# Kernel optimization log

Measured on AMD Instinct MI355X. Metric: run time of the kernel, lower is better.

## Reference

```python
import jax, jax.numpy as jnp
import numpy as np

EPS = 1e-5
NUM_HEADS = 8
KEY_DIM = 32
V_DIM = 128  # att_ratio * key_dim

def bn2d(x, g, b, m, v):
    # inference BatchNorm2d on NCHW
    s = g * jax.lax.rsqrt(v + EPS)
    return x * s[None, :, None, None] + (b - m * s)[None, :, None, None]

def conv1x1(x, w):
    # w: [out_c, in_c], x: [B,C,H,W]
    return jnp.einsum('oc,bchw->bohw', w, x)

def _bn_params(key, c):
    k1, k2, k3, k4 = jax.random.split(key, 4)
    g = jax.random.uniform(k1, (c,), jnp.float32, 0.5, 1.5)
    b = jax.random.normal(k2, (c,), jnp.float32) * 0.1
    m = jax.random.normal(k3, (c,), jnp.float32) * 0.1
    v = jax.random.uniform(k4, (c,), jnp.float32, 0.5, 1.5)
    return g, b, m, v

def setup_inputs() -> dict:
    key = jax.random.key(0)
    ks = jax.random.split(key, 12)
    inp_dim, out_dim = 256, 512
    kv_out = (KEY_DIM + V_DIM) * NUM_HEADS      # 1280
    q_out = KEY_DIM * NUM_HEADS                 # 256
    merge_dim = V_DIM * NUM_HEADS               # 1024
    hid = out_dim * 2                            # mlp_ratio=2 -> 1024
    d = {}
    d['x'] = jax.random.normal(ks[0], (32, inp_dim, 32, 32), jnp.float32)
    d['kv_w'] = jax.random.normal(ks[1], (kv_out, inp_dim), jnp.float32) * 0.02
    d['kv_g'], d['kv_b'], d['kv_m'], d['kv_v'] = _bn_params(ks[2], kv_out)
    d['q_w'] = jax.random.normal(ks[3], (q_out, inp_dim), jnp.float32) * 0.02
    d['q_g'], d['q_b'], d['q_m'], d['q_v'] = _bn_params(ks[4], q_out)
    d['mg_w'] = jax.random.normal(ks[5], (out_dim, merge_dim), jnp.float32) * 0.02
    d['mg_g'], d['mg_b'], d['mg_m'], d['mg_v'] = _bn_params(ks[6], out_dim)
    d['fc1_w'] = jax.random.normal(ks[7], (hid, out_dim), jnp.float32) * 0.02
    d['bn1_g'], d['bn1_b'], d['bn1_m'], d['bn1_v'] = _bn_params(ks[8], hid)
    d['fc2_w'] = jax.random.normal(ks[9], (out_dim, hid), jnp.float32) * 0.02
    d['bn2_g'], d['bn2_b'], d['bn2_m'], d['bn2_v'] = _bn_params(ks[10], out_dim)
    return d

def reference(x, kv_w, kv_g, kv_b, kv_m, kv_v, q_w, q_g, q_b, q_m, q_v,
              mg_w, mg_g, mg_b, mg_m, mg_v,
              fc1_w, bn1_g, bn1_b, bn1_m, bn1_v,
              fc2_w, bn2_g, bn2_b, bn2_m, bn2_v):
    B, C, H, W = x.shape
    scale = KEY_DIM ** (-0.5)
    # kv projection: conv1x1 + BN, then split per head into k, v
    kv = bn2d(conv1x1(x, kv_w), kv_g, kv_b, kv_m, kv_v)
    kv = kv.reshape(B, NUM_HEADS, KEY_DIM + V_DIM, H * W)
    k = kv[:, :, :KEY_DIM]   # [B,h,Dk,N]
    v = kv[:, :, KEY_DIM:]   # [B,h,Dv,N]
    # query subsampling: AvgPool2d(kernel=1, stride=2) == strided slice
    xq = x[:, :, ::2, ::2]
    q = bn2d(conv1x1(xq, q_w), q_g, q_b, q_m, q_v)
    q = q.reshape(B, NUM_HEADS, KEY_DIM, -1)  # [B,h,Dk,Nq]
    # att = q^T @ k * scale, softmax over keys
    att = jax.nn.softmax(jnp.einsum('bhdq,bhdn->bhqn', q, k) * scale, axis=-1)
    h2, w2 = (H + 1) // 2, (W + 1) // 2
    # out = v @ att^T, channel-first layout
    o = jnp.einsum('bhvn,bhqn->bhvq', v, att).reshape(B, NUM_HEADS * V_DIM, h2, w2)
    # merge: GELU -> conv1x1 -> BN
    o = bn2d(conv1x1(jax.nn.gelu(o, approximate=False), mg_w), mg_g, mg_b, mg_m, mg_v)
    # ConvMlp: conv1x1 -> BN -> GELU -> conv1x1 -> BN
    y = bn2d(conv1x1(o, fc1_w), bn1_g, bn1_b, bn1_m, bn1_v)
    y = jax.nn.gelu(y, approximate=False)
    y = bn2d(conv1x1(y, fc2_w), bn2_g, bn2_b, bn2_m, bn2_v)
    return y
```

## Files before the change

kernel.cpp:

```cpp
#include <hip/hip_runtime.h>
#include <hip/hip_bf16.h>

#define BN_EPS 1e-5f

typedef short s8v __attribute__((ext_vector_type(8)));
typedef float f4v __attribute__((ext_vector_type(4)));
typedef unsigned short u16x8 __attribute__((ext_vector_type(8)));

__device__ __forceinline__ float bu2f(unsigned short u) {
    union { unsigned int i; float f; } c; c.i = ((unsigned int)u) << 16; return c.f;
}
__device__ __forceinline__ unsigned short f2bu(float f) {
    union { float f; unsigned int i; } c; c.f = f;
    unsigned int i = c.i;
    i += 0x7FFFu + ((i >> 16) & 1u);
    return (unsigned short)(i >> 16);
}
__device__ __forceinline__ float gelu_exact(float x) {
    return 0.5f * x * (1.0f + erff(x * 0.70710678118654752f));
}
__device__ __forceinline__ float ldin(const void* p, long i, bool f32) {
    return f32 ? ((const float*)p)[i] : bu2f(((const unsigned short*)p)[i]);
}
__device__ __forceinline__ s8v ldfrag(const unsigned short* p) {
    return *reinterpret_cast<const s8v*>(p);
}
__device__ __forceinline__ void gld16(const void* g, void* l) {
    __builtin_amdgcn_global_load_lds(
        (const __attribute__((address_space(1))) unsigned int*)g,
        (__attribute__((address_space(3))) unsigned int*)l, 16, 0, 0);
}
__device__ __forceinline__ s8v ldsw32(const unsigned short* T, int row, int quad) {
    return *reinterpret_cast<const s8v*>(T + row * 32 + ((quad ^ ((row >> 1) & 3)) << 3));
}
__device__ __forceinline__ s8v ldsw64(const unsigned short* T, int row, int chunk) {
    return *reinterpret_cast<const s8v*>(T + row * 64 + ((chunk ^ (row & 7)) << 3));
}
__device__ __forceinline__ int detect_f32(const unsigned short* xu) {
    int insane = 0;
    for (int i = 0; i < 128; ++i) {
        unsigned int e = (xu[i] >> 7) & 0xFFu;
        if (e == 255u || (e != 0u && (e < 96u || e > 159u))) ++insane;
    }
    return (insane >= 16) ? 1 : 0;
}

__global__ __launch_bounds__(256)
void prep_kernel(const void* __restrict__ x,
                 const void* __restrict__ w0, const void* __restrict__ w1,
                 const void* __restrict__ w2, const void* __restrict__ w3,
                 const void* __restrict__ w4,
                 unsigned short* __restrict__ wdst,
                 unsigned short* __restrict__ xT,
                 unsigned short* __restrict__ xqT,
                 int* __restrict__ dtf)
{
    __shared__ int sflag;
    __shared__ unsigned short T[64][66];
    const int tid = threadIdx.x;
    const int bid = blockIdx.x;
    if (tid == 0) {
        int fl = detect_f32((const unsigned short*)x);
        sflag = fl;
        if (bid == 0) *dtf = fl;
    }
    __syncthreads();
    const bool f = (sflag != 0);

    if (bid < 960) {
        long idx = (long)bid * 2048 + tid * 8;
        const void* s; long off;
        if      (idx <  327680L) { s = w0; off = idx; }
        else if (idx <  393216L) { s = w1; off = idx - 327680L; }
        else if (idx <  917504L) { s = w2; off = idx - 393216L; }
        else if (idx < 1441792L) { s = w3; off = idx - 917504L; }
        else                     { s = w4; off = idx - 1441792L; }
        u16x8 pk;
        if (f) {
            float4 a = *((const float4*)((const float*)s + off));
            float4 b = *((const float4*)((const float*)s + off + 4));
            pk[0]=f2bu(a.x); pk[1]=f2bu(a.y); pk[2]=f2bu(a.z); pk[3]=f2bu(a.w);
            pk[4]=f2bu(b.x); pk[5]=f2bu(b.y); pk[6]=f2bu(b.z); pk[7]=f2bu(b.w);
        } else {
            pk = *((const u16x8*)((const unsigned short*)s + off));
        }
        *reinterpret_cast<u16x8*>(wdst + idx) = pk;
        return;
    }
    int b, c0, n0, ND; bool SUBS;
    if (bid < 3008) { int t = bid - 960;  b = t >> 6; int r = t & 63;
                      c0 = (r >> 4) * 64; n0 = (r & 15) * 64; ND = 1024; SUBS = false; }
    else            { int t = bid - 3008; b = t >> 4; int r = t & 15;
                      c0 = (r >> 2) * 64; n0 = (r & 3) * 64;  ND = 256;  SUBS = true; }
    unsigned short* dst = SUBS ? xqT : xT;
    {
        int nn = tid & 63, cq = tid >> 6;
        int n = n0 + nn;
        int sc = SUBS ? ((n >> 4) * 64 + (n & 15) * 2) : n;
        long base = ((long)b * 256 + c0 + cq * 16) * 1024 + sc;
        #pragma unroll
        for (int i = 0; i < 16; ++i)
            T[nn][cq * 16 + i] = f2bu(ldin(x, base + (long)i * 1024, f));
    }
    __syncthreads();
    {
        int cc = tid & 63, nq = tid >> 6;
        #pragma unroll
        for (int i = 0; i < 16; ++i) {
            int nn = nq * 16 + i;
            dst[((long)b * ND + n0 + nn) * 256 + c0 + cc] = T[nn][cc];
        }
    }
}

template<int OUT_MODE, bool DO_GELU, bool PRESCALE, int BM>
__global__ __launch_bounds__(256)
void mfma_gemm(const unsigned short* __restrict__ A,
               const unsigned short* __restrict__ B,
               const void* __restrict__ gg, const void* __restrict__ bb,
               const void* __restrict__ mmu, const void* __restrict__ vv,
               void* __restrict__ out0, unsigned short* __restrict__ out1,
               int M, int K, int N, const int* __restrict__ dtflag)
{
    constexpr int NF = (BM == 128) ? 4 : 2;
    __shared__ unsigned short As[BM * 64];
    __shared__ unsigned short Bs[128 * 64];
    __shared__ float sS[BM], sO[BM];

    const bool wf = (*dtflag != 0);
    const int tid = threadIdx.x;
    const int lane = tid & 63;
    const int wave = tid >> 6;
    const int quad = lane >> 4;
    const int l15  = lane & 15;
    const int wm2 = (BM == 128) ? (wave >> 1) * 64 : 0;
    const int wn2 = (BM == 128) ? (wave & 1) * 64 : wave * 32;
    const int b  = blockIdx.z;
    const int bm = blockIdx.y * BM;
    const int bn = blockIdx.x * 128;

    if (tid < BM) {
        int m = bm + tid;
        float g  = ldin(gg,  m, wf), be = ldin(bb,  m, wf);
        float mu = ldin(mmu, m, wf), va = ldin(vv,  m, wf);
        float s = g * rsqrtf(va + BN_EPS);
        float o = be - mu * s;
        if (PRESCALE) { s *= 0.17677669529663687f; o *= 0.17677669529663687f; }
        sS[tid] = s; sO[tid] = o;
    }

    const unsigned short* Bb = B + (long)b * N * K;

    f4v acc[4][NF];
    #pragma unroll
    for (int i = 0; i < 4; ++i)
        #pragma unroll
        for (int j = 0; j < NF; ++j) acc[i][j] = (f4v){0.f, 0.f, 0.f, 0.f};

    const int lr8 = lane >> 3;
    const int lc8 = lane & 7;

    for (int k0 = 0; k0 < K; k0 += 64) {
        #pragma unroll
        for (int j = 0; j < (BM == 128 ? 4 : 2); ++j) {
            int base = wave * (BM == 128 ? 32 : 16) + j * 8;
            int r = base + lr8;
            gld16(A + (long)(bm + r) * K + k0 + ((lc8 ^ (r & 7)) << 3),
                  As + base * 64);
        }
        #pragma unroll
        for (int j = 0; j < 4; ++j) {
            int base = wave * 32 + j * 8;
            int r = base + lr8;
            gld16(Bb + (long)(bn + r) * K + k0 + ((lc8 ^ (r & 7)) << 3),
                  Bs + base * 64);
        }
        __syncthreads();

        #pragma unroll
        for (int sk = 0; sk < 2; ++sk) {
            s8v af[4], bfr[NF];
            #pragma unroll
            for (int i = 0; i < 4; ++i)
                af[i]  = ldsw64(As, wm2 + i * 16 + l15, sk * 4 + quad);
            #pragma unroll
            for (int j = 0; j < NF; ++j)
                bfr[j] = ldsw64(Bs, wn2 + j * 16 + l15, sk * 4 + quad);
            #pragma unroll
            for (int i = 0; i < 4; ++i)
                #pragma unroll
                for (int j = 0; j < NF; ++j)
                    acc[i][j] = __builtin_amdgcn_mfma_f32_16x16x32_bf16(
                        af[i], bfr[j], acc[i][j], 0, 0, 0);
        }
        __syncthreads();
    }

    #pragma unroll
    for (int i = 0; i < 4; ++i) {
        int m0l = wm2 + i * 16 + quad * 4;
        int m0  = bm + m0l;
        float s0 = sS[m0l + 0], o0 = sO[m0l + 0];
        float s1 = sS[m0l + 1], o1 = sO[m0l + 1];
        float s2 = sS[m0l + 2], o2 = sO[m0l + 2];
        float s3 = sS[m0l + 3], o3 = sO[m0l + 3];
        #pragma unroll
        for (int j = 0; j < NF; ++j) {
            int n = bn + wn2 + j * 16 + l15;
            float v0 = acc[i][j][0] * s0 + o0;
            float v1 = acc[i][j][1] * s1 + o1;
            float v2 = acc[i][j][2] * s2 + o2;
            float v3 = acc[i][j][3] * s3 + o3;
            if (DO_GELU) {
                v0 = gelu_exact(v0); v1 = gelu_exact(v1);
                v2 = gelu_exact(v2); v3 = gelu_exact(v3);
            }
            if (OUT_MODE == 0) {
                ushort4 pk; pk.x = f2bu(v0); pk.y = f2bu(v1);
                pk.z = f2bu(v2); pk.w = f2bu(v3);
                *reinterpret_cast<ushort4*>(
                    (unsigned short*)out0 + ((long)b * N + n) * M + m0) = pk;
            } else if (OUT_MODE == 1) {
                int h = m0 / 160, seg = m0 - h * 160;
                if (seg < 32) {
                    ushort4 pk; pk.x = f2bu(v0); pk.y = f2bu(v1);
                    pk.z = f2bu(v2); pk.w = f2bu(v3);
                    *reinterpret_cast<ushort4*>(
                        (unsigned short*)out0 + ((long)(b * 8 + h) * 1024 + n) * 32 + seg) = pk;
                } else {
                    long vb = (((long)b * 8 + h) * 128 + (seg - 32)) * N + n;
                    out1[vb + 0 * N] = f2bu(v0);
                    out1[vb + 1 * N] = f2bu(v1);
                    out1[vb + 2 * N] = f2bu(v2);
                    out1[vb + 3 * N] = f2bu(v3);
                }
            } else if (OUT_MODE == 2) {
                int b2 = n >> 8, nl = n & 255;
                long ob = ((long)b2 * M + m0) * 256 + nl;
                if (wf) {
                    ((float*)out0)[ob + 0L * 256] = v0;
                    ((float*)out0)[ob + 1L * 256] = v1;
                    ((float*)out0)[ob + 2L * 256] = v2;
                    ((float*)out0)[ob + 3L * 256] = v3;
                } else {
                    ((unsigned short*)out0)[ob + 0L * 256] = f2bu(v0);
                    ((unsigned short*)out0)[ob + 1L * 256] = f2bu(v1);
                    ((unsigned short*)out0)[ob + 2L * 256] = f2bu(v2);
                    ((unsigned short*)out0)[ob + 3L * 256] = f2bu(v3);
                }
            } else {
                int h = m0 >> 5;
                ushort4 pk; pk.x = f2bu(v0); pk.y = f2bu(v1);
                pk.z = f2bu(v2); pk.w = f2bu(v3);
                *reinterpret_cast<ushort4*>(
                    (unsigned short*)out0 + ((long)(b * 8 + h) * 256 + n) * 32 + (m0 & 31)) = pk;
            }
        }
    }
}

__global__ __launch_bounds__(512, 4)
void attn_mfma(const unsigned short* __restrict__ kvK,
               const unsigned short* __restrict__ kvV,
               const unsigned short* __restrict__ qh,
               unsigned short* __restrict__ goT)
{
    __shared__ unsigned short Ks[64 * 32];
    __shared__ unsigned short Vs[128 * 64];
    __shared__ unsigned short Ps[128][72];
    __shared__ float redS[128];

    const int tid = threadIdx.x;
    const int lane = tid & 63;
    const int wave = tid >> 6;
    const int quad = lane >> 4;
    const int l15  = lane & 15;
    const int h    = blockIdx.x;
    const int b    = blockIdx.y;
    const int q0   = blockIdx.z * 128;
    const int wq   = wave * 16;

    const unsigned short* Qb = qh  + (long)(b * 8 + h) * 256 * 32;
    const unsigned short* Kb = kvK + (long)(b * 8 + h) * 1024 * 32;
    const unsigned short* Vb = kvV + (long)(b * 8 + h) * 128 * 1024;

    s8v qf = ldfrag(Qb + (long)(q0 + wq + l15) * 32 + quad * 8);

    f4v o[8];
    #pragma unroll
    for (int i = 0; i < 8; ++i) o[i] = (f4v){0.f, 0.f, 0.f, 0.f};
    float rs[4] = {0.f, 0.f, 0.f, 0.f};

    for (int n0 = 0; n0 < 1024; n0 += 64) {
        if (wave < 4) {
            int r = wave * 16 + (lane >> 2);
            int c = (lane & 3) ^ ((r >> 1) & 3);
            gld16(Kb + (long)(n0 + r) * 32 + (c << 3), Ks + wave * 16 * 32);
        }
        {
            int rb = wave * 16;
            int r0 = rb + (lane >> 3), r1 = r0 + 8;
            int s  = lane & 7;
            gld16(Vb + (long)r0 * 1024 + n0 + ((s ^ (r0 & 7)) << 3), Vs + rb * 64);
            gld16(Vb + (long)r1 * 1024 + n0 + ((s ^ (r1 & 7)) << 3), Vs + (rb + 8) * 64);
        }
        __syncthreads();

        #pragma unroll
        for (int j = 0; j < 4; ++j) {
            s8v kf = ldsw32(Ks, j * 16 + l15, quad);
            f4v z = (f4v){0.f, 0.f, 0.f, 0.f};
            f4v sa = __builtin_amdgcn_mfma_f32_16x16x32_bf16(qf, kf, z, 0, 0, 0);
            #pragma unroll
            for (int r = 0; r < 4; ++r) {
                float p = __expf(fminf(sa[r], 30.f));
                rs[r] += p;
                Ps[wq + quad * 4 + r][j * 16 + l15] = f2bu(p);
            }
        }
        #pragma unroll
        for (int ks = 0; ks < 2; ++ks) {
            s8v pf = ldfrag(&Ps[wq + l15][ks * 32 + quad * 8]);
            #pragma unroll
            for (int i = 0; i < 8; ++i) {
                s8v vf = ldsw64(Vs, i * 16 + l15, ks * 4 + quad);
                o[i] = __builtin_amdgcn_mfma_f32_16x16x32_bf16(vf, pf, o[i], 0, 0, 0);
            }
        }
        __syncthreads();
    }

    #pragma unroll
    for (int r = 0; r < 4; ++r) {
        float s = rs[r];
        s += __shfl_xor(s, 1);
        s += __shfl_xor(s, 2);
        s += __shfl_xor(s, 4);
        s += __shfl_xor(s, 8);
        if (l15 == 0) redS[wq + quad * 4 + r] = s;
    }
    float linv = 1.0f / redS[wq + l15];
    int q = q0 + wq + l15;
    #pragma unroll
    for (int i = 0; i < 8; ++i) {
        ushort4 pk;
        pk.x = f2bu(gelu_exact(o[i][0] * linv));
        pk.y = f2bu(gelu_exact(o[i][1] * linv));
        pk.z = f2bu(gelu_exact(o[i][2] * linv));
        pk.w = f2bu(gelu_exact(o[i][3] * linv));
        *reinterpret_cast<ushort4*>(
            goT + ((long)b * 256 + q) * 1024 + h * 128 + i * 16 + quad * 4) = pk;
    }
}

extern "C" void kernel_launch(void* const* d_in, const int* in_sizes, int n_in,
                              void* d_out, int out_size, void* d_ws, size_t ws_size,
                              hipStream_t stream)
{
    const void* x     = d_in[0];
    const void* kv_w  = d_in[1];
    const void* kv_g  = d_in[2];  const void* kv_b  = d_in[3];
    const void* kv_m  = d_in[4];  const void* kv_v  = d_in[5];
    const void* q_w   = d_in[6];
    const void* q_g   = d_in[7];  const void* q_b   = d_in[8];
    const void* q_m   = d_in[9];  const void* q_v   = d_in[10];
    const void* mg_w  = d_in[11];
    const void* mg_g  = d_in[12]; const void* mg_b  = d_in[13];
    const void* mg_m  = d_in[14]; const void* mg_v  = d_in[15];
    const void* fc1_w = d_in[16];
    const void* bn1_g = d_in[17]; const void* bn1_b = d_in[18];
    const void* bn1_m = d_in[19]; const void* bn1_v = d_in[20];
    const void* fc2_w = d_in[21];
    const void* bn2_g = d_in[22]; const void* bn2_b = d_in[23];
    const void* bn2_m = d_in[24]; const void* bn2_v = d_in[25];

    unsigned short* ws  = (unsigned short*)d_ws;
    int*            dtf = (int*)d_ws;
    unsigned short* wsW  = ws + 8;
    unsigned short* wKV  = wsW;
    unsigned short* wQ   = wsW + 327680L;
    unsigned short* wMG  = wsW + 393216L;
    unsigned short* wFC1 = wsW + 917504L;
    unsigned short* wFC2 = wsW + 1441792L;
    unsigned short* xT   = ws + 1966088L;
    unsigned short* goT  = xT;
    unsigned short* xqT  = ws + 10354696L;
    unsigned short* qhb  = ws + 12451848L;
    unsigned short* kvK  = ws + 14549000L;
    unsigned short* kvV  = ws + 22937608L;
    unsigned short* y1T  = kvV;
    unsigned short* y2T  = kvV + 4194304L;

    dim3 blk(256, 1, 1);

    prep_kernel<<<3520, blk, 0, stream>>>(
        x, kv_w, q_w, mg_w, fc1_w, fc2_w, wsW, xT, xqT, dtf);

    mfma_gemm<3, false, true, 64><<<dim3(2, 4, 32), blk, 0, stream>>>(
        wQ, xqT, q_g, q_b, q_m, q_v, qhb, nullptr, 256, 256, 256, dtf);

    mfma_gemm<1, false, false, 128><<<dim3(8, 10, 32), blk, 0, stream>>>(
        wKV, xT, kv_g, kv_b, kv_m, kv_v, kvK, kvV, 1280, 256, 1024, dtf);

    attn_mfma<<<dim3(8, 32, 2), dim3(512, 1, 1), 0, stream>>>(kvK, kvV, qhb, goT);

    mfma_gemm<0, false, false, 64><<<dim3(64, 8, 1), blk, 0, stream>>>(
        wMG, goT, mg_g, mg_b, mg_m, mg_v, y1T, nullptr, 512, 1024, 8192, dtf);

    mfma_gemm<0, true, false, 64><<<dim3(64, 16, 1), blk, 0, stream>>>(
        wFC1, y1T, bn1_g, bn1_b, bn1_m, bn1_v, y2T, nullptr, 1024, 512, 8192, dtf);

    mfma_gemm<2, false, false, 64><<<dim3(64, 8, 1), blk, 0, stream>>>(
        wFC2, y2T, bn2_g, bn2_b, bn2_m, bn2_v, d_out, nullptr, 512, 1024, 8192, dtf);
}
```

Baseline: 307.8 us.

## Split KV projection into K and V GEMMs with LDS-staged coalesced stores

Reorders the KV weight rows during prep so all K rows and all V rows are contiguous. The KV projection then runs as two kernels: the K part uses the generic GEMM with remapped BN parameters, and a new V GEMM swaps operand roles and transposes its tile through LDS. Both write 16-byte coalesced rows, replacing the scalar strided V stores. The generic GEMM also stages its mode 0/3 epilogue through a shared-memory tile for wide stores, and sets a minimum occupancy hint. This adds a kernel launch and extra LDS traffic plus barriers in the epilogue.

```diff
diff --git a/kernel.cpp b/kernel.cpp
--- a/kernel.cpp
+++ b/kernel.cpp
@@ -70,7 +70,13 @@
     if (bid < 960) {
         long idx = (long)bid * 2048 + tid * 8;
         const void* s; long off;
-        if      (idx <  327680L) { s = w0; off = idx; }
+        if (idx < 65536L) {
+            long rk = idx >> 8;
+            s = w0; off = ((rk >> 5) * 160 + (rk & 31)) * 256 + (idx & 255);
+        } else if (idx < 327680L) {
+            long rv = (idx - 65536L) >> 8;
+            s = w0; off = ((rv >> 7) * 160 + 32 + (rv & 127)) * 256 + (idx & 255);
+        }
         else if (idx <  393216L) { s = w1; off = idx - 327680L; }
         else if (idx <  917504L) { s = w2; off = idx - 393216L; }
         else if (idx < 1441792L) { s = w3; off = idx - 917504L; }
@@ -113,19 +119,20 @@
     }
 }
 
-template<int OUT_MODE, bool DO_GELU, bool PRESCALE, int BM>
-__global__ __launch_bounds__(256)
+template<int OUT_MODE, bool DO_GELU, bool PRESCALE, bool REMAPK>
+__global__ __launch_bounds__(256, 4)
 void mfma_gemm(const unsigned short* __restrict__ A,
                const unsigned short* __restrict__ B,
                const void* __restrict__ gg, const void* __restrict__ bb,
                const void* __restrict__ mmu, const void* __restrict__ vv,
-               void* __restrict__ out0, unsigned short* __restrict__ out1,
+               void* __restrict__ out0,
                int M, int K, int N, const int* __restrict__ dtflag)
 {
-    constexpr int NF = (BM == 128) ? 4 : 2;
-    __shared__ unsigned short As[BM * 64];
-    __shared__ unsigned short Bs[128 * 64];
-    __shared__ float sS[BM], sO[BM];
+    __shared__ union {
+        struct { unsigned short As[64 * 64]; unsigned short Bs[128 * 64]; } s;
+        unsigned short tile[128 * 68];
+    } u;
+    __shared__ float sS[64], sO[64];
 
     const bool wf = (*dtflag != 0);
     const int tid = threadIdx.x;
@@ -133,16 +140,16 @@
     const int wave = tid >> 6;
     const int quad = lane >> 4;
     const int l15  = lane & 15;
-    const int wm2 = (BM == 128) ? (wave >> 1) * 64 : 0;
-    const int wn2 = (BM == 128) ? (wave & 1) * 64 : wave * 32;
+    const int wn2 = wave * 32;
     const int b  = blockIdx.z;
-    const int bm = blockIdx.y * BM;
+    const int bm = blockIdx.y * 64;
     const int bn = blockIdx.x * 128;
 
-    if (tid < BM) {
+    if (tid < 64) {
         int m = bm + tid;
-        float g  = ldin(gg,  m, wf), be = ldin(bb,  m, wf);
-        float mu = ldin(mmu, m, wf), va = ldin(vv,  m, wf);
+        int mo = REMAPK ? ((m >> 5) * 160 + (m & 31)) : m;
+        float g  = ldin(gg,  mo, wf), be = ldin(bb,  mo, wf);
+        float mu = ldin(mmu, mo, wf), va = ldin(vv,  mo, wf);
         float s = g * rsqrtf(va + BN_EPS);
         float o = be - mu * s;
         if (PRESCALE) { s *= 0.17677669529663687f; o *= 0.17677669529663687f; }
@@ -151,90 +158,101 @@
 
     const unsigned short* Bb = B + (long)b * N * K;
 
-    f4v acc[4][NF];
+    f4v acc[4][2];
     #pragma unroll
     for (int i = 0; i < 4; ++i)
         #pragma unroll
-        for (int j = 0; j < NF; ++j) acc[i][j] = (f4v){0.f, 0.f, 0.f, 0.f};
+        for (int j = 0; j < 2; ++j) acc[i][j] = (f4v){0.f, 0.f, 0.f, 0.f};
 
     const int lr8 = lane >> 3;
     const int lc8 = lane & 7;
 
     for (int k0 = 0; k0 < K; k0 += 64) {
         #pragma unroll
-        for (int j = 0; j < (BM == 128 ? 4 : 2); ++j) {
-            int base = wave * (BM == 128 ? 32 : 16) + j * 8;
+        for (int j = 0; j < 2; ++j) {
+            int base = wave * 16 + j * 8;
             int r = base + lr8;
             gld16(A + (long)(bm + r) * K + k0 + ((lc8 ^ (r & 7)) << 3),
-                  As + base * 64);
+                  u.s.As + base * 64);
         }
         #pragma unroll
         for (int j = 0; j < 4; ++j) {
             int base = wave * 32 + j * 8;
             int r = base + lr8;
             gld16(Bb + (long)(bn + r) * K + k0 + ((lc8 ^ (r & 7)) << 3),
-                  Bs + base * 64);
+                  u.s.Bs + base * 64);
         }
         __syncthreads();
 
         #pragma unroll
         for (int sk = 0; sk < 2; ++sk) {
-            s8v af[4], bfr[NF];
+            s8v af[4], bfr[2];
             #pragma unroll
             for (int i = 0; i < 4; ++i)
-                af[i]  = ldsw64(As, wm2 + i * 16 + l15, sk * 4 + quad);
-            #pragma unroll
-            for (int j = 0; j < NF; ++j)
-                bfr[j] = ldsw64(Bs, wn2 + j * 16 + l15, sk * 4 + quad);
+                af[i]  = ldsw64(u.s.As, i * 16 + l15, sk * 4 + quad);
+            #pragma unroll
+            for (int j = 0; j < 2; ++j)
+                bfr[j] = ldsw64(u.s.Bs, wn2 + j * 16 + l15, sk * 4 + quad);
             #pragma unroll
             for (int i = 0; i < 4; ++i)
                 #pragma unroll
-                for (int j = 0; j < NF; ++j)
+                for (int j = 0; j < 2; ++j)
                     acc[i][j] = __builtin_amdgcn_mfma_f32_16x16x32_bf16(
                         af[i], bfr[j], acc[i][j], 0, 0, 0);
         }
         __syncthreads();
     }
 
-    #pragma unroll
-    for (int i = 0; i < 4; ++i) {
-        int m0l = wm2 + i * 16 + quad * 4;
-        int m0  = bm + m0l;
-        float s0 = sS[m0l + 0], o0 = sO[m0l + 0];
-        float s1 = sS[m0l + 1], o1 = sO[m0l + 1];
-        float s2 = sS[m0l + 2], o2 = sO[m0l + 2];
-        float s3 = sS[m0l + 3], o3 = sO[m0l + 3];
-        #pragma unroll
-        for (int j = 0; j < NF; ++j) {
-            int n = bn + wn2 + j * 16 + l15;
-            float v0 = acc[i][j][0] * s0 + o0;
-            float v1 = acc[i][j][1] * s1 + o1;
-            float v2 = acc[i][j][2] * s2 + o2;
-            float v3 = acc[i][j][3] * s3 + o3;
-            if (DO_GELU) {
-                v0 = gelu_exact(v0); v1 = gelu_exact(v1);
-                v2 = gelu_exact(v2); v3 = gelu_exact(v3);
+    if (OUT_MODE == 0 || OUT_MODE == 3) {
+        #pragma unroll
+        for (int j = 0; j < 2; ++j) {
+            int n = wn2 + j * 16 + l15;
+            #pragma unroll
+            for (int i = 0; i < 4; ++i) {
+                int mcol = i * 16 + quad * 4;
+                ushort4 pk;
+                float v0 = acc[i][j][0] * sS[mcol + 0] + sO[mcol + 0];
+                float v1 = acc[i][j][1] * sS[mcol + 1] + sO[mcol + 1];
+                float v2 = acc[i][j][2] * sS[mcol + 2] + sO[mcol + 2];
+                float v3 = acc[i][j][3] * sS[mcol + 3] + sO[mcol + 3];
+                if (DO_GELU) {
+                    v0 = gelu_exact(v0); v1 = gelu_exact(v1);
+                    v2 = gelu_exact(v2); v3 = gelu_exact(v3);
+                }
+                pk.x = f2bu(v0); pk.y = f2bu(v1); pk.z = f2bu(v2); pk.w = f2bu(v3);
+                *reinterpret_cast<ushort4*>(&u.tile[n * 68 + mcol]) = pk;
             }
+        }
+        __syncthreads();
+        #pragma unroll
+        for (int p = 0; p < 4; ++p) {
+            int n = p * 32 + (tid >> 3), c = tid & 7;
+            u16x8 val = *reinterpret_cast<const u16x8*>(&u.tile[n * 68 + c * 8]);
             if (OUT_MODE == 0) {
-                ushort4 pk; pk.x = f2bu(v0); pk.y = f2bu(v1);
-                pk.z = f2bu(v2); pk.w = f2bu(v3);
-                *reinterpret_cast<ushort4*>(
-                    (unsigned short*)out0 + ((long)b * N + n) * M + m0) = pk;
-            } else if (OUT_MODE == 1) {
-                int h = m0 / 160, seg = m0 - h * 160;
-                if (seg < 32) {
-                    ushort4 pk; pk.x = f2bu(v0); pk.y = f2bu(v1);
-                    pk.z = f2bu(v2); pk.w = f2bu(v3);
-                    *reinterpret_cast<ushort4*>(
-                        (unsigned short*)out0 + ((long)(b * 8 + h) * 1024 + n) * 32 + seg) = pk;
-                } else {
-                    long vb = (((long)b * 8 + h) * 128 + (seg - 32)) * N + n;
-                    out1[vb + 0 * N] = f2bu(v0);
-                    out1[vb + 1 * N] = f2bu(v1);
-                    out1[vb + 2 * N] = f2bu(v2);
-                    out1[vb + 3 * N] = f2bu(v3);
-                }
-            } else if (OUT_MODE == 2) {
+                *reinterpret_cast<u16x8*>(
+                    (unsigned short*)out0 + ((long)b * N + bn + n) * M + bm + c * 8) = val;
+            } else {
+                int m = bm + c * 8, h = m >> 5;
+                *reinterpret_cast<u16x8*>(
+                    (unsigned short*)out0 + (((long)b * 8 + h) * N + bn + n) * 32 + (m & 31)) = val;
+            }
+        }
+    } else {
+        #pragma unroll
+        for (int i = 0; i < 4; ++i) {
+            int m0l = i * 16 + quad * 4;
+            int m0  = bm + m0l;
+            float s0 = sS[m0l + 0], o0 = sO[m0l + 0];
+            float s1 = sS[m0l + 1], o1 = sO[m0l + 1];
+            float s2 = sS[m0l + 2], o2 = sO[m0l + 2];
+            float s3 = sS[m0l + 3], o3 = sO[m0l + 3];
+            #pragma unroll
+            for (int j = 0; j < 2; ++j) {
+                int n = bn + wn2 + j * 16 + l15;
+                float v0 = acc[i][j][0] * s0 + o0;
+                float v1 = acc[i][j][1] * s1 + o1;
+                float v2 = acc[i][j][2] * s2 + o2;
+                float v3 = acc[i][j][3] * s3 + o3;
                 int b2 = n >> 8, nl = n & 255;
                 long ob = ((long)b2 * M + m0) * 256 + nl;
                 if (wf) {
@@ -248,14 +266,110 @@
                     ((unsigned short*)out0)[ob + 2L * 256] = f2bu(v2);
                     ((unsigned short*)out0)[ob + 3L * 256] = f2bu(v3);
                 }
-            } else {
-                int h = m0 >> 5;
-                ushort4 pk; pk.x = f2bu(v0); pk.y = f2bu(v1);
-                pk.z = f2bu(v2); pk.w = f2bu(v3);
-                *reinterpret_cast<ushort4*>(
-                    (unsigned short*)out0 + ((long)(b * 8 + h) * 256 + n) * 32 + (m0 & 31)) = pk;
             }
         }
+    }
+}
+
+__global__ __launch_bounds__(256, 4)
+void kvv_gemm(const unsigned short* __restrict__ xT,
+              const unsigned short* __restrict__ wV,
+              const void* __restrict__ gg, const void* __restrict__ bb,
+              const void* __restrict__ mmu, const void* __restrict__ vv,
+              unsigned short* __restrict__ kvV, const int* __restrict__ dtflag)
+{
+    __shared__ union {
+        struct { unsigned short As[128 * 64]; unsigned short Bs[128 * 64]; } s;
+        unsigned short VT[128 * 132];
+    } u;
+    __shared__ float sS[128], sO[128];
+
+    const bool wf = (*dtflag != 0);
+    const int tid = threadIdx.x;
+    const int lane = tid & 63;
+    const int wave = tid >> 6;
+    const int quad = lane >> 4;
+    const int l15  = lane & 15;
+    const int wm2 = (wave >> 1) * 64;
+    const int wn2 = (wave & 1) * 64;
+    const int b  = blockIdx.z;
+    const int bv = blockIdx.x * 128;
+    const int bk = blockIdx.y * 128;
+
+    if (tid < 128) {
+        int vg = bv + tid;
+        int mo = (vg >> 7) * 160 + 32 + (vg & 127);
+        float g  = ldin(gg,  mo, wf), be = ldin(bb,  mo, wf);
+        float mu = ldin(mmu, mo, wf), va = ldin(vv,  mo, wf);
+        float s = g * rsqrtf(va + BN_EPS);
+        sS[tid] = s; sO[tid] = be - mu * s;
+    }
+
+    const unsigned short* Xb = xT + (long)b * 1024 * 256;
+
+    f4v acc[4][4];
+    #pragma unroll
+    for (int i = 0; i < 4; ++i)
+        #pragma unroll
+        for (int j = 0; j < 4; ++j) acc[i][j] = (f4v){0.f, 0.f, 0.f, 0.f};
+
+    const int lr8 = lane >> 3;
+    const int lc8 = lane & 7;
+
+    for (int k0 = 0; k0 < 256; k0 += 64) {
+        #pragma unroll
+        for (int j = 0; j < 4; ++j) {
+            int base = wave * 32 + j * 8;
+            int r = base + lr8;
+            gld16(Xb + (long)(bk + r) * 256 + k0 + ((lc8 ^ (r & 7)) << 3),
+                  u.s.As + base * 64);
+            gld16(wV + (long)(bv + r) * 256 + k0 + ((lc8 ^ (r & 7)) << 3),
+                  u.s.Bs + base * 64);
+        }
+        __syncthreads();
+
+        #pragma unroll
+        for (int sk = 0; sk < 2; ++sk) {
+            s8v af[4], bfr[4];
+            #pragma unroll
+            for (int i = 0; i < 4; ++i)
+                af[i]  = ldsw64(u.s.As, wm2 + i * 16 + l15, sk * 4 + quad);
+            #pragma unroll
+            for (int j = 0; j < 4; ++j)
+                bfr[j] = ldsw64(u.s.Bs, wn2 + j * 16 + l15, sk * 4 + quad);
+            #pragma unroll
+            for (int i = 0; i < 4; ++i)
+                #pragma unroll
+                for (int j = 0; j < 4; ++j)
+                    acc[i][j] = __builtin_amdgcn_mfma_f32_16x16x32_bf16(
+                        af[i], bfr[j], acc[i][j], 0, 0, 0);
+        }
+        __syncthreads();
+    }
+
+    #pragma unroll
+    for (int j = 0; j < 4; ++j) {
+        int vloc = wn2 + j * 16 + l15;
+        float s = sS[vloc], o = sO[vloc];
+        #pragma unroll
+        for (int i = 0; i < 4; ++i) {
+            int kcol = wm2 + i * 16 + quad * 4;
+            ushort4 pk;
+            pk.x = f2bu(acc[i][j][0] * s + o);
+            pk.y = f2bu(acc[i][j][1] * s + o);
+            pk.z = f2bu(acc[i][j][2] * s + o);
+            pk.w = f2bu(acc[i][j][3] * s + o);
+            *reinterpret_cast<ushort4*>(&u.VT[vloc * 132 + kcol]) = pk;
+        }
+    }
+    __syncthreads();
+    const int h = bv >> 7;
+    #pragma unroll
+    for (int p = 0; p < 8; ++p) {
+        int vloc = p * 16 + (tid >> 4), c = tid & 15;
+        u16x8 val = *reinterpret_cast<const u16x8*>(&u.VT[vloc * 132 + c * 8]);
+        *reinterpret_cast<u16x8*>(
+            kvV + (((long)b * 8 + h) * 128 + (bv & 127) + vloc) * 1024 + bk + c * 8) = val;
     }
 }
 
@@ -377,7 +491,8 @@
     unsigned short* ws  = (unsigned short*)d_ws;
     int*            dtf = (int*)d_ws;
     unsigned short* wsW  = ws + 8;
-    unsigned short* wKV  = wsW;
+    unsigned short* wKVk = wsW;
+    unsigned short* wKVv = wsW + 65536L;
     unsigned short* wQ   = wsW + 327680L;
     unsigned short* wMG  = wsW + 393216L;
     unsigned short* wFC1 = wsW + 917504L;
@@ -396,20 +511,23 @@
     prep_kernel<<<3520, blk, 0, stream>>>(
         x, kv_w, q_w, mg_w, fc1_w, fc2_w, wsW, xT, xqT, dtf);
 
-    mfma_gemm<3, false, true, 64><<<dim3(2, 4, 32), blk, 0, stream>>>(
-        wQ, xqT, q_g, q_b, q_m, q_v, qhb, nullptr, 256, 256, 256, dtf);
-
-    mfma_gemm<1, false, false, 128><<<dim3(8, 10, 32), blk, 0, stream>>>(
-        wKV, xT, kv_g, kv_b, kv_m, kv_v, kvK, kvV, 1280, 256, 1024, dtf);
+    mfma_gemm<3, false, true, false><<<dim3(2, 4, 32), blk, 0, stream>>>(
+        wQ, xqT, q_g, q_b, q_m, q_v, qhb, 256, 256, 256, dtf);
+
+    mfma_gemm<3, false, false, true><<<dim3(8, 4, 32), blk, 0, stream>>>(
+        wKVk, xT, kv_g, kv_b, kv_m, kv_v, kvK, 256, 256, 1024, dtf);
+
+    kvv_gemm<<<dim3(8, 8, 32), blk, 0, stream>>>(
+        xT, wKVv, kv_g, kv_b, kv_m, kv_v, kvV, dtf);
 
     attn_mfma<<<dim3(8, 32, 2), dim3(512, 1, 1), 0, stream>>>(kvK, kvV, qhb, goT);
 
-    mfma_gemm<0, false, false, 64><<<dim3(64, 8, 1), blk, 0, stream>>>(
-        wMG, goT, mg_g, mg_b, mg_m, mg_v, y1T, nullptr, 512, 1024, 8192, dtf);
-
-    mfma_gemm<0, true, false, 64><<<dim3(64, 16, 1), blk, 0, stream>>>(
-        wFC1, y1T, bn1_g, bn1_b, bn1_m, bn1_v, y2T, nullptr, 1024, 512, 8192, dtf);
-
-    mfma_gemm<2, false, false, 64><<<dim3(64, 8, 1), blk, 0, stream>>>(
-        wFC2, y2T, bn2_g, bn2_b, bn2_m, bn2_v, d_out, nullptr, 512, 1024, 8192, dtf);
-}
+    mfma_gemm<0, false, false, false><<<dim3(64, 8, 1), blk, 0, stream>>>(
+        wMG, goT, mg_g, mg_b, mg_m, mg_v, y1T, 512, 1024, 8192, dtf);
+
+    mfma_gemm<0, true, false, false><<<dim3(64, 16, 1), blk, 0, stream>>>(
+        wFC1, y1T, bn1_g, bn1_b, bn1_m, bn1_v, y2T, 1024, 512, 8192, dtf);
+
+    mfma_gemm<2, false, false, false><<<dim3(64, 8, 1), blk, 0, stream>>>(
+        wFC2, y2T, bn2_g, bn2_b, bn2_m, bn2_v, d_out, 512, 1024, 8192, dtf);
+}
```

New measurement: 316.7 us. +2.9%, slower.
